# Performance work log

Measured on AMD Instinct MI355X. Metric: run time of the kernel, lower is better.

## Reference

```python
import jax, jax.numpy as jnp
import numpy as np
import math

D_MODEL = 1024
H = 16
D_K = D_MODEL // H
D_FF = 4096
NEG = -1e9


def layer_norm(x, alpha, bias):
    # Faithful to source: mean over last dim, UNBIASED std (torch.std default),
    # eps defined in source but never used in forward.
    mean = jnp.mean(x, axis=-1, keepdims=True)
    std = jnp.std(x, axis=-1, ddof=1, keepdims=True)
    return (x - mean) / std * alpha + bias


def mha(x, mask, w_q, w_k, w_v, w_o):
    B, S, D = x.shape
    q = (x @ w_q.T).reshape(B, S, H, D_K)
    k = (x @ w_k.T).reshape(B, S, H, D_K)
    v = (x @ w_v.T).reshape(B, S, H, D_K)
    scores = jnp.einsum('bqhd,bkhd->bhqk', q, k) / math.sqrt(D_K)
    scores = jnp.where(mask, NEG, scores)
    attn = jax.nn.softmax(scores, axis=-1)
    out = jnp.einsum('bhqk,bkhd->bqhd', attn, v).reshape(B, S, D)
    return out @ w_o.T


def setup_inputs() -> dict:
    key = jax.random.key(0)
    ks = jax.random.split(key, 16)
    B, S = 4, 2048
    s = 0.02
    return {
        'x': jax.random.normal(ks[0], (B, S, D_MODEL), jnp.float32),
        'w_q': jax.random.normal(ks[1], (D_MODEL, D_MODEL), jnp.float32) * s,
        'w_k': jax.random.normal(ks[2], (D_MODEL, D_MODEL), jnp.float32) * s,
        'w_v': jax.random.normal(ks[3], (D_MODEL, D_MODEL), jnp.float32) * s,
        'w_o': jax.random.normal(ks[4], (D_MODEL, D_MODEL), jnp.float32) * s,
        'l1_w': jax.random.normal(ks[5], (D_FF, D_MODEL), jnp.float32) * s,
        'l1_b': jnp.zeros((D_FF,), jnp.float32),
        'l2_w': jax.random.normal(ks[6], (D_MODEL, D_FF), jnp.float32) * s,
        'l2_b': jnp.zeros((D_MODEL,), jnp.float32),
        'norm1_a': jnp.ones((D_MODEL,), jnp.float32),
        'norm1_b': jnp.zeros((D_MODEL,), jnp.float32),
        'norm2_a': jnp.ones((D_MODEL,), jnp.float32),
        'norm2_b': jnp.zeros((D_MODEL,), jnp.float32),
        'normf_a': jnp.ones((D_MODEL,), jnp.float32),
        'normf_b': jnp.zeros((D_MODEL,), jnp.float32),
        'mask': jax.random.randint(ks[7], (B, 1, 1, S), 0, 2) == 1,
    }


def reference(x, w_q, w_k, w_v, w_o, l1_w, l1_b, l2_w, l2_b,
              norm1_a, norm1_b, norm2_a, norm2_b, normf_a, normf_b, mask):
    # residual 1: pre-norm self-attention (dropout is identity at eval)
    x = x + mha(layer_norm(x, norm1_a, norm1_b), mask, w_q, w_k, w_v, w_o)
    # residual 2: pre-norm FFN
    h = layer_norm(x, norm2_a, norm2_b)
    ff = jax.nn.relu(h @ l1_w.T + l1_b) @ l2_w.T + l2_b
    x = x + ff
    return layer_norm(x, normf_a, normf_b)
```

## Files before the change

kernel.cpp:

```cpp
#include <hip/hip_runtime.h>
#include <hip/hip_bf16.h>


typedef __bf16 bf16x8 __attribute__((ext_vector_type(8)));
typedef float f32x4 __attribute__((ext_vector_type(4)));
typedef unsigned short u16x8 __attribute__((ext_vector_type(8)));
using bf16 = __hip_bfloat16;

__device__ __forceinline__ f32x4 mfma16(bf16x8 a, bf16x8 b, f32x4 c) {
  return __builtin_amdgcn_mfma_f32_16x16x32_bf16(a, b, c, 0, 0, 0);
}

__device__ __forceinline__ int swz(int row, int blk) {
  return row * 64 + ((blk ^ (row & 7)) << 3);
}

__device__ __forceinline__ void stage_tile64(unsigned short* lds,
                                             const bf16* g, int ld, int rows) {
  const int lane = threadIdx.x & 63, wid = threadIdx.x >> 6;
  const int r8 = lane >> 3, blk = lane & 7;
  const bf16* gl = g + (size_t)r8 * ld + ((blk ^ r8) << 3);
  const int passes = rows >> 3;
  for (int p = wid; p < passes; p += 4) {
    __builtin_amdgcn_global_load_lds(
        (const __attribute__((address_space(1))) void*)(gl + (size_t)(p * 8) * ld),
        (__attribute__((address_space(3))) void*)(lds + p * 512),
        16, 0, 0);
  }
}

__device__ __forceinline__ short bfb(float x) {
  return (short)__hip_bfloat16_raw(__float2bfloat16(x)).x;
}

__global__ __launch_bounds__(256) void cvt_k(const float* __restrict__ s,
                                             bf16* __restrict__ d, int n) {
  const int i = (blockIdx.x * 256 + threadIdx.x) * 4;
  if (i + 3 < n) {
    const float4 v = *reinterpret_cast<const float4*>(s + i);
    ushort4 o;
    o.x = (unsigned short)bfb(v.x);
    o.y = (unsigned short)bfb(v.y);
    o.z = (unsigned short)bfb(v.z);
    o.w = (unsigned short)bfb(v.w);
    *reinterpret_cast<ushort4*>(d + i) = o;
  }
}

template <bool OUT_F32>
__global__ __launch_bounds__(256) void layernorm_k(const float* __restrict__ in,
                                                   const float* __restrict__ gamma,
                                                   const float* __restrict__ beta,
                                                   void* __restrict__ out) {
  __shared__ float red[8];
  const int row = blockIdx.x, t = threadIdx.x;
  const float4 vv = reinterpret_cast<const float4*>(in + (size_t)row * 1024)[t];
  const float x0 = vv.x, x1 = vv.y, x2 = vv.z, x3 = vv.w;
  float s = x0 + x1 + x2 + x3;
#pragma unroll
  for (int off = 32; off; off >>= 1) s += __shfl_down(s, off);
  if ((t & 63) == 0) red[t >> 6] = s;
  __syncthreads();
  const float mean = (red[0] + red[1] + red[2] + red[3]) * (1.0f / 1024.0f);
  const float d0 = x0 - mean, d1 = x1 - mean, d2 = x2 - mean, d3 = x3 - mean;
  float sq = d0 * d0 + d1 * d1 + d2 * d2 + d3 * d3;
#pragma unroll
  for (int off = 32; off; off >>= 1) sq += __shfl_down(sq, off);
  if ((t & 63) == 0) red[4 + (t >> 6)] = sq;
  __syncthreads();
  const float var =
      fmaxf((red[4] + red[5] + red[6] + red[7]) * (1.0f / 1023.0f), 1e-20f);
  const float rstd = rsqrtf(var);
  const float4 ga = reinterpret_cast<const float4*>(gamma)[t];
  const float4 be = reinterpret_cast<const float4*>(beta)[t];
  const float y0 = d0 * rstd * ga.x + be.x;
  const float y1 = d1 * rstd * ga.y + be.y;
  const float y2 = d2 * rstd * ga.z + be.z;
  const float y3 = d3 * rstd * ga.w + be.w;
  if (OUT_F32) {
    reinterpret_cast<float4*>((float*)out + (size_t)row * 1024)[t] =
        make_float4(y0, y1, y2, y3);
  } else {
    ushort4 o;
    o.x = (unsigned short)bfb(y0);
    o.y = (unsigned short)bfb(y1);
    o.z = (unsigned short)bfb(y2);
    o.w = (unsigned short)bfb(y3);
    reinterpret_cast<ushort4*>((bf16*)out + (size_t)row * 1024)[t] = o;
  }
}

template <bool HAS_BIAS, bool RELU, bool HAS_RES, bool OUT_F32>
__global__ __launch_bounds__(256) void gemm_bt(const bf16* __restrict__ A,
                                               const bf16* __restrict__ W,
                                               const float* __restrict__ bias,
                                               const float* __restrict__ resid,
                                               void* __restrict__ out,
                                               int M, int N, int K,
                                               int lda, int ldw) {
  __shared__ __align__(16) unsigned short As[128 * 64];
  __shared__ __align__(16) unsigned short Bs[128 * 64];
  const int lane = threadIdx.x & 63, wid = threadIdx.x >> 6;
  const int n16 = lane & 15, quad = lane >> 4;
  const int wm = (wid >> 1) * 64, wn = (wid & 1) * 64;
  const int tm = blockIdx.x * 128, tn = blockIdx.y * 128;
  f32x4 acc[4][4] = {};
  for (int k0 = 0; k0 < K; k0 += 64) {
    stage_tile64(As, A + (size_t)tm * lda + k0, lda, 128);
    stage_tile64(Bs, W + (size_t)tn * ldw + k0, ldw, 128);
    __syncthreads();
#pragma unroll
    for (int kk = 0; kk < 64; kk += 32) {
      bf16x8 af[4], bw[4];
#pragma unroll
      for (int i = 0; i < 4; ++i)
        af[i] = *reinterpret_cast<const bf16x8*>(
            &As[swz(wm + i * 16 + n16, (kk >> 3) + quad)]);
#pragma unroll
      for (int j = 0; j < 4; ++j)
        bw[j] = *reinterpret_cast<const bf16x8*>(
            &Bs[swz(wn + j * 16 + n16, (kk >> 3) + quad)]);
#pragma unroll
      for (int i = 0; i < 4; ++i)
#pragma unroll
        for (int j = 0; j < 4; ++j) acc[i][j] = mfma16(af[i], bw[j], acc[i][j]);
    }
    __syncthreads();
  }
#pragma unroll
  for (int i = 0; i < 4; ++i) {
#pragma unroll
    for (int j = 0; j < 4; ++j) {
      const int n = tn + wn + j * 16 + n16;
      const float bv = HAS_BIAS ? bias[n] : 0.0f;
#pragma unroll
      for (int r = 0; r < 4; ++r) {
        const int m = tm + wm + i * 16 + quad * 4 + r;
        float vv = acc[i][j][r] + bv;
        if (RELU) vv = fmaxf(vv, 0.0f);
        if (HAS_RES) vv += resid[(size_t)m * N + n];
        if (OUT_F32)
          ((float*)out)[(size_t)m * N + n] = vv;
        else
          ((bf16*)out)[(size_t)m * N + n] = __float2bfloat16(vv);
      }
    }
  }
}

__global__ __launch_bounds__(256) void prep_mask_k(const int* __restrict__ m,
                                                   float* __restrict__ mf,
                                                   int n) {
  __shared__ int s;
  if (threadIdx.x == 0) s = 0;
  __syncthreads();
  unsigned int acc = 0;
  for (int i = threadIdx.x; i < 512; i += 256)
    acc |= ((const unsigned int*)m)[i] & 0xFFFFFF00u;
  if (acc) atomicOr(&s, 1);
  __syncthreads();
  const bool bytes = (s != 0);
  const int i = blockIdx.x * 256 + threadIdx.x;
  if (i < n) {
    const int v = bytes ? (int)((const unsigned char*)m)[i] : m[i];
    mf[i] = v ? -1.4427e9f : 0.0f;
  }
}

__global__ __launch_bounds__(256) void scan_k(const float* __restrict__ maskf,
                                              float* __restrict__ cmask,
                                              int* __restrict__ idx,
                                              int* __restrict__ cnt) {
  __shared__ int wsum[4];
  const int b = blockIdx.x, t = threadIdx.x, lane = t & 63, w = t >> 6;
  const float* mrow = maskf + b * 2048;
  int keep[8], local = 0;
#pragma unroll
  for (int e = 0; e < 8; ++e) {
    keep[e] = (mrow[t * 8 + e] == 0.0f) ? 1 : 0;
    local += keep[e];
  }
  int inc = local;
#pragma unroll
  for (int off = 1; off < 64; off <<= 1) {
    int v = __shfl_up(inc, off);
    if (lane >= off) inc += v;
  }
  if (lane == 63) wsum[w] = inc;
  __syncthreads();
  int base = 0;
#pragma unroll
  for (int i = 0; i < 4; ++i)
    if (i < w) base += wsum[i];
  int p = base + inc - local;
#pragma unroll
  for (int e = 0; e < 8; ++e)
    if (keep[e]) idx[b * 2048 + p++] = t * 8 + e;
  const int total = wsum[0] + wsum[1] + wsum[2] + wsum[3];
  if (t == 0) cnt[b] = total;
  for (int i = t; i < 2048; i += 256)
    cmask[b * 2048 + i] = (i < total) ? 0.0f : -1.4427e9f;
}

__global__ __launch_bounds__(256) void gather_k(const bf16* __restrict__ qkv,
                                                const int* __restrict__ idx,
                                                const int* __restrict__ cnt,
                                                bf16* __restrict__ kv) {
  const int b = blockIdx.x >> 11, j = blockIdx.x & 2047;
  const int n = cnt[b];
  const int npad = (n + 63) & ~63;
  if (j >= npad) return;
  u16x8* dst = reinterpret_cast<u16x8*>(kv + ((size_t)(b * 2048 + j)) * 2048);
  if (j < n) {
    const int s = idx[b * 2048 + j];
    const u16x8* src = reinterpret_cast<const u16x8*>(
        qkv + ((size_t)(b * 2048 + s)) * 3072 + 1024);
    dst[threadIdx.x] = src[threadIdx.x];
  } else {
    u16x8 z = {};
    dst[threadIdx.x] = z;
  }
}

__global__ __launch_bounds__(256) void attn_k(const bf16* __restrict__ qkv,
                                              const bf16* __restrict__ kv,
                                              const float* __restrict__ cmask,
                                              const int* __restrict__ cnt,
                                              bf16* __restrict__ out, int BHN) {
  __shared__ __align__(16) unsigned short Ks[2][64 * 64];
  __shared__ __align__(16) unsigned short Vs[2][64 * 72];
  const int lane = threadIdx.x & 63, wid = threadIdx.x >> 6;
  const int n16 = lane & 15, quad = lane >> 4;
  const int bid = blockIdx.x;
  const int bh = bid % BHN, qb = bid / BHN;
  const int b = bh >> 4, h = bh & 15;
  const size_t rowb = (size_t)b * 2048 * 3072;
  const bf16* qp0 = qkv + rowb + h * 64;
  const bf16* kp0 = kv + (size_t)b * 2048 * 2048 + h * 64;
  const bf16* vp0 = kp0 + 1024;
  const float* mfb = cmask + b * 2048;
  const int nk = ((cnt[b] + 63) >> 6) << 6;
  const int qrow0 = qb * 128 + wid * 32;

  bf16x8 qf[2][2];
#pragma unroll
  for (int g = 0; g < 2; ++g) {
    const bf16* qp = qp0 + (size_t)(qrow0 + g * 16 + n16) * 3072 + quad * 8;
    qf[g][0] = *reinterpret_cast<const bf16x8*>(qp);
    qf[g][1] = *reinterpret_cast<const bf16x8*>(qp + 32);
  }
  bf16x8 ones;
#pragma unroll
  for (int e = 0; e < 8; ++e) ones[e] = (__bf16)1.0f;
  f32x4 oacc[2][4] = {};
  f32x4 lacc[2] = {};
  const int prow = ((n16 >> 2) << 3) + (n16 & 3);
  const int vkey = lane, vdc = wid * 16;

  stage_tile64(Ks[0], kp0, 2048, 64);
  {
    const bf16* vp = vp0 + (size_t)vkey * 2048 + vdc;
    const u16x8 a = *reinterpret_cast<const u16x8*>(vp);
    const u16x8 bq = *reinterpret_cast<const u16x8*>(vp + 8);
#pragma unroll
    for (int e = 0; e < 8; ++e) {
      Vs[0][(vdc + e) * 72 + vkey] = a[e];
      Vs[0][(vdc + 8 + e) * 72 + vkey] = bq[e];
    }
  }
  int cur = 0;
  for (int kt = 0; kt < nk; kt += 64) {
    __syncthreads();
    const bool hasNext = (kt + 64 < nk);
    u16x8 na = {}, nb = {};
    if (hasNext) {
      stage_tile64(Ks[cur ^ 1], kp0 + (size_t)(kt + 64) * 2048, 2048, 64);
      const bf16* vp = vp0 + (size_t)(kt + 64 + vkey) * 2048 + vdc;
      na = *reinterpret_cast<const u16x8*>(vp);
      nb = *reinterpret_cast<const u16x8*>(vp + 8);
    }
    const unsigned short* Kc = Ks[cur];
    const unsigned short* Vc = Vs[cur];
#pragma unroll
    for (int sub = 0; sub < 2; ++sub) {
      const int kb = sub * 32;
      bf16x8 aflo[2], afhi[2];
#pragma unroll
      for (int st = 0; st < 2; ++st) {
        const int row = kb + prow + st * 4;
        aflo[st] = *reinterpret_cast<const bf16x8*>(&Kc[swz(row, quad)]);
        afhi[st] = *reinterpret_cast<const bf16x8*>(&Kc[swz(row, 4 + quad)]);
      }
      __builtin_amdgcn_s_setprio(1);
      f32x4 z[2][2];
#pragma unroll
      for (int g = 0; g < 2; ++g)
#pragma unroll
        for (int st = 0; st < 2; ++st) {
          f32x4 zz = {};
          zz = mfma16(aflo[st], qf[g][0], zz);
          zz = mfma16(afhi[st], qf[g][1], zz);
          z[g][st] = zz;
        }
      __builtin_amdgcn_s_setprio(0);
      const float4 m0 =
          *reinterpret_cast<const float4*>(mfb + kt + kb + quad * 8);
      const float4 m1 =
          *reinterpret_cast<const float4*>(mfb + kt + kb + quad * 8 + 4);
      bf16x8 vf[4];
#pragma unroll
      for (int j = 0; j < 4; ++j)
        vf[j] = *reinterpret_cast<const bf16x8*>(
            &Vc[(j * 16 + n16) * 72 + kb + quad * 8]);
#pragma unroll
      for (int g = 0; g < 2; ++g) {
        bf16x8 pf;
#pragma unroll
        for (int r = 0; r < 4; ++r) {
          const float e0 = __builtin_amdgcn_exp2f(
              fmaf(z[g][0][r], 0.18033688f, ((const float*)&m0)[r]));
          const float e1 = __builtin_amdgcn_exp2f(
              fmaf(z[g][1][r], 0.18033688f, ((const float*)&m1)[r]));
          pf[r] = (__bf16)e0;
          pf[4 + r] = (__bf16)e1;
        }
        __builtin_amdgcn_s_setprio(1);
#pragma unroll
        for (int j = 0; j < 4; ++j) oacc[g][j] = mfma16(pf, vf[j], oacc[g][j]);
        lacc[g] = mfma16(pf, ones, lacc[g]);
        __builtin_amdgcn_s_setprio(0);
      }
    }
    if (hasNext) {
      unsigned short* Vn = Vs[cur ^ 1];
#pragma unroll
      for (int e = 0; e < 8; ++e) {
        Vn[(vdc + e) * 72 + vkey] = na[e];
        Vn[(vdc + 8 + e) * 72 + vkey] = nb[e];
      }
    }
    cur ^= 1;
  }
#pragma unroll
  for (int g = 0; g < 2; ++g) {
#pragma unroll
    for (int r = 0; r < 4; ++r) {
      const float lr = 1.0f / fmaxf(lacc[g][r], 1e-20f);
      bf16* op =
          out + (size_t)(b * 2048 + qrow0 + g * 16 + quad * 4 + r) * 1024 +
          h * 64;
#pragma unroll
      for (int j = 0; j < 4; ++j)
        op[j * 16 + n16] = __float2bfloat16(oacc[g][j][r] * lr);
    }
  }
}

extern "C" void kernel_launch(void* const* d_in, const int* in_sizes, int n_in,
                              void* d_out, int out_size, void* d_ws,
                              size_t ws_size, hipStream_t stream) {
  const float* x    = (const float*)d_in[0];
  const float* w_q  = (const float*)d_in[1];
  const float* w_k  = (const float*)d_in[2];
  const float* w_v  = (const float*)d_in[3];
  const float* w_o  = (const float*)d_in[4];
  const float* l1_w = (const float*)d_in[5];
  const float* l1_b = (const float*)d_in[6];
  const float* l2_w = (const float*)d_in[7];
  const float* l2_b = (const float*)d_in[8];
  const float* n1a  = (const float*)d_in[9];
  const float* n1b  = (const float*)d_in[10];
  const float* n2a  = (const float*)d_in[11];
  const float* n2b  = (const float*)d_in[12];
  const float* nfa  = (const float*)d_in[13];
  const float* nfb  = (const float*)d_in[14];
  const int* mask   = (const int*)d_in[15];

  const int D = 1024, FF = 4096;
  const int M = in_sizes[0] / D;
  const int B = M / 2048;

  const size_t MB = 1024ull * 1024ull;
  if (ws_size < 121 * MB) return;
  char* w = (char*)d_ws;
  bf16* WQKV = (bf16*)(w + 0 * MB);
  bf16* WO   = (bf16*)(w + 6 * MB);
  bf16* L1W  = (bf16*)(w + 8 * MB);
  bf16* L2W  = (bf16*)(w + 16 * MB);
  bf16* LN1  = (bf16*)(w + 24 * MB);
  bf16* QKV  = (bf16*)(w + 40 * MB);
  bf16* ATT  = LN1;
  bf16* HLN  = (bf16*)(w + 40 * MB);
  bf16* FF1  = (bf16*)(w + 56 * MB);
  bf16* KV   = (bf16*)(w + 88 * MB);
  float* X1  = (float*)(w + 88 * MB);
  float* MASKF = (float*)(w + 120 * MB);
  float* CMASK = (float*)(w + 120 * MB + 256 * 1024);
  int*   IDX   = (int*)(w + 120 * MB + 512 * 1024);
  int*   CNT   = (int*)(w + 120 * MB + 768 * 1024);

  const dim3 blk(256);
  cvt_k<<<dim3(D * D / 1024), blk, 0, stream>>>(w_q, WQKV, D * D);
  cvt_k<<<dim3(D * D / 1024), blk, 0, stream>>>(w_k, WQKV + D * D, D * D);
  cvt_k<<<dim3(D * D / 1024), blk, 0, stream>>>(w_v, WQKV + 2 * D * D, D * D);
  cvt_k<<<dim3(D * D / 1024), blk, 0, stream>>>(w_o, WO, D * D);
  cvt_k<<<dim3(FF * D / 1024), blk, 0, stream>>>(l1_w, L1W, FF * D);
  cvt_k<<<dim3(FF * D / 1024), blk, 0, stream>>>(l2_w, L2W, FF * D);
  prep_mask_k<<<dim3((M + 255) / 256), blk, 0, stream>>>(mask, MASKF, M);
  scan_k<<<dim3(B), blk, 0, stream>>>(MASKF, CMASK, IDX, CNT);

  layernorm_k<false><<<M, blk, 0, stream>>>(x, n1a, n1b, LN1);
  gemm_bt<false, false, false, false>
      <<<dim3(M / 128, 3072 / 128), blk, 0, stream>>>(LN1, WQKV, nullptr,
                                                      nullptr, QKV, M, 3072, D,
                                                      D, D);
  gather_k<<<dim3(B * 2048), blk, 0, stream>>>(QKV, IDX, CNT, KV);
  const int BHN = B * 16;
  attn_k<<<dim3((M / 128) * 16), blk, 0, stream>>>(QKV, KV, CMASK, CNT, ATT,
                                                   BHN);
  gemm_bt<false, false, true, true><<<dim3(M / 128, D / 128), blk, 0, stream>>>(
      ATT, WO, nullptr, x, X1, M, D, D, D, D);
  layernorm_k<false><<<M, blk, 0, stream>>>(X1, n2a, n2b, HLN);
  for (int c = 0; c < 2; ++c) {
    gemm_bt<true, true, false, false>
        <<<dim3(M / 128, 2048 / 128), blk, 0, stream>>>(
            HLN, L1W + (size_t)c * 2048 * D, l1_b + c * 2048, nullptr, FF1, M,
            2048, D, D, D);
    if (c == 0)
      gemm_bt<true, false, true, true>
          <<<dim3(M / 128, D / 128), blk, 0, stream>>>(
              FF1, L2W + c * 2048, l2_b, X1, X1, M, D, 2048, 2048, FF);
    else
      gemm_bt<false, false, true, true>
          <<<dim3(M / 128, D / 128), blk, 0, stream>>>(
              FF1, L2W + c * 2048, nullptr, X1, X1, M, D, 2048, 2048, FF);
  }
  layernorm_k<true><<<M, blk, 0, stream>>>(X1, nfa, nfb, (float*)d_out);
}
```

Before: 520.1 us.

## Gather unmasked LN rows before K/V projection and skip padded GEMM tiles

The fused QKV projection is split in two. Q is computed for all rows, while the layernormed input is first gathered to the unmasked key positions and only those rows go through the K/V GEMM. Workgroups whose rows fall past the padded count exit early, so masked keys never pay for the K/V projection. GEMM tiles are also remapped across groups of eight for locality, and attention skips the mask loads on fully valid key tiles. The cost is an extra kernel launch and a gather of LN rows, and the padding granularity changes to 128.

```diff
diff --git a/kernel.cpp b/kernel.cpp
--- a/kernel.cpp
+++ b/kernel.cpp
@@ -90,20 +90,34 @@
   }
 }
 
-template <bool HAS_BIAS, bool RELU, bool HAS_RES, bool OUT_F32>
+template <bool HAS_BIAS, bool RELU, bool HAS_RES, bool OUT_F32, bool KV_EXIT>
 __global__ __launch_bounds__(256) void gemm_bt(const bf16* __restrict__ A,
                                                const bf16* __restrict__ W,
                                                const float* __restrict__ bias,
                                                const float* __restrict__ resid,
                                                void* __restrict__ out,
                                                int M, int N, int K,
-                                               int lda, int ldw) {
+                                               int lda, int ldw,
+                                               const int* __restrict__ cnt) {
   __shared__ __align__(16) unsigned short As[128 * 64];
   __shared__ __align__(16) unsigned short Bs[128 * 64];
+  int bx = blockIdx.x, by = blockIdx.y;
+  const int nwg = gridDim.x * gridDim.y;
+  if ((nwg & 7) == 0) {
+    const int lid = by * gridDim.x + bx;
+    const int cpx = nwg >> 3;
+    const int s = (lid & 7) * cpx + (lid >> 3);
+    bx = s % gridDim.x;
+    by = s / gridDim.x;
+  }
+  const int tm = bx * 128, tn = by * 128;
+  if (KV_EXIT) {
+    const int npad = (cnt[tm >> 11] + 127) & ~127;
+    if ((tm & 2047) >= npad) return;
+  }
   const int lane = threadIdx.x & 63, wid = threadIdx.x >> 6;
   const int n16 = lane & 15, quad = lane >> 4;
   const int wm = (wid >> 1) * 64, wn = (wid & 1) * 64;
-  const int tm = blockIdx.x * 128, tn = blockIdx.y * 128;
   f32x4 acc[4][4] = {};
   for (int k0 = 0; k0 < K; k0 += 64) {
     stage_tile64(As, A + (size_t)tm * lda + k0, lda, 128);
@@ -202,19 +216,19 @@
     cmask[b * 2048 + i] = (i < total) ? 0.0f : -1.4427e9f;
 }
 
-__global__ __launch_bounds__(256) void gather_k(const bf16* __restrict__ qkv,
-                                                const int* __restrict__ idx,
-                                                const int* __restrict__ cnt,
-                                                bf16* __restrict__ kv) {
+__global__ __launch_bounds__(128) void gatherA_k(const bf16* __restrict__ ln1,
+                                                 const int* __restrict__ idx,
+                                                 const int* __restrict__ cnt,
+                                                 bf16* __restrict__ cln) {
   const int b = blockIdx.x >> 11, j = blockIdx.x & 2047;
   const int n = cnt[b];
-  const int npad = (n + 63) & ~63;
+  const int npad = (n + 127) & ~127;
   if (j >= npad) return;
-  u16x8* dst = reinterpret_cast<u16x8*>(kv + ((size_t)(b * 2048 + j)) * 2048);
+  u16x8* dst = reinterpret_cast<u16x8*>(cln + ((size_t)(b * 2048 + j)) * 1024);
   if (j < n) {
     const int s = idx[b * 2048 + j];
-    const u16x8* src = reinterpret_cast<const u16x8*>(
-        qkv + ((size_t)(b * 2048 + s)) * 3072 + 1024);
+    const u16x8* src =
+        reinterpret_cast<const u16x8*>(ln1 + ((size_t)(b * 2048 + s)) * 1024);
     dst[threadIdx.x] = src[threadIdx.x];
   } else {
     u16x8 z = {};
@@ -222,7 +236,7 @@
   }
 }
 
-__global__ __launch_bounds__(256) void attn_k(const bf16* __restrict__ qkv,
+__global__ __launch_bounds__(256) void attn_k(const bf16* __restrict__ q,
                                               const bf16* __restrict__ kv,
                                               const float* __restrict__ cmask,
                                               const int* __restrict__ cnt,
@@ -234,18 +248,18 @@
   const int bid = blockIdx.x;
   const int bh = bid % BHN, qb = bid / BHN;
   const int b = bh >> 4, h = bh & 15;
-  const size_t rowb = (size_t)b * 2048 * 3072;
-  const bf16* qp0 = qkv + rowb + h * 64;
+  const bf16* qp0 = q + (size_t)b * 2048 * 1024 + h * 64;
   const bf16* kp0 = kv + (size_t)b * 2048 * 2048 + h * 64;
   const bf16* vp0 = kp0 + 1024;
   const float* mfb = cmask + b * 2048;
-  const int nk = ((cnt[b] + 63) >> 6) << 6;
+  const int cntb = cnt[b];
+  const int nk = ((cntb + 63) >> 6) << 6;
   const int qrow0 = qb * 128 + wid * 32;
 
   bf16x8 qf[2][2];
 #pragma unroll
   for (int g = 0; g < 2; ++g) {
-    const bf16* qp = qp0 + (size_t)(qrow0 + g * 16 + n16) * 3072 + quad * 8;
+    const bf16* qp = qp0 + (size_t)(qrow0 + g * 16 + n16) * 1024 + quad * 8;
     qf[g][0] = *reinterpret_cast<const bf16x8*>(qp);
     qf[g][1] = *reinterpret_cast<const bf16x8*>(qp + 32);
   }
@@ -272,6 +286,7 @@
   for (int kt = 0; kt < nk; kt += 64) {
     __syncthreads();
     const bool hasNext = (kt + 64 < nk);
+    const bool fullTile = (kt + 64 <= cntb);
     u16x8 na = {}, nb = {};
     if (hasNext) {
       stage_tile64(Ks[cur ^ 1], kp0 + (size_t)(kt + 64) * 2048, 2048, 64);
@@ -303,10 +318,12 @@
           z[g][st] = zz;
         }
       __builtin_amdgcn_s_setprio(0);
-      const float4 m0 =
-          *reinterpret_cast<const float4*>(mfb + kt + kb + quad * 8);
-      const float4 m1 =
-          *reinterpret_cast<const float4*>(mfb + kt + kb + quad * 8 + 4);
+      float4 m0 = make_float4(0.f, 0.f, 0.f, 0.f);
+      float4 m1 = make_float4(0.f, 0.f, 0.f, 0.f);
+      if (!fullTile) {
+        m0 = *reinterpret_cast<const float4*>(mfb + kt + kb + quad * 8);
+        m1 = *reinterpret_cast<const float4*>(mfb + kt + kb + quad * 8 + 4);
+      }
       bf16x8 vf[4];
 #pragma unroll
       for (int j = 0; j < 4; ++j)
@@ -388,9 +405,10 @@
   bf16* L1W  = (bf16*)(w + 8 * MB);
   bf16* L2W  = (bf16*)(w + 16 * MB);
   bf16* LN1  = (bf16*)(w + 24 * MB);
-  bf16* QKV  = (bf16*)(w + 40 * MB);
+  bf16* Qbuf = (bf16*)(w + 40 * MB);
   bf16* ATT  = LN1;
   bf16* HLN  = (bf16*)(w + 40 * MB);
+  bf16* CLN  = (bf16*)(w + 56 * MB);
   bf16* FF1  = (bf16*)(w + 56 * MB);
   bf16* KV   = (bf16*)(w + 88 * MB);
   float* X1  = (float*)(w + 88 * MB);
@@ -410,30 +428,37 @@
   scan_k<<<dim3(B), blk, 0, stream>>>(MASKF, CMASK, IDX, CNT);
 
   layernorm_k<false><<<M, blk, 0, stream>>>(x, n1a, n1b, LN1);
-  gemm_bt<false, false, false, false>
-      <<<dim3(M / 128, 3072 / 128), blk, 0, stream>>>(LN1, WQKV, nullptr,
-                                                      nullptr, QKV, M, 3072, D,
-                                                      D, D);
-  gather_k<<<dim3(B * 2048), blk, 0, stream>>>(QKV, IDX, CNT, KV);
+  gemm_bt<false, false, false, false, false>
+      <<<dim3(M / 128, D / 128), blk, 0, stream>>>(LN1, WQKV, nullptr, nullptr,
+                                                   Qbuf, M, D, D, D, D,
+                                                   nullptr);
+  gatherA_k<<<dim3(B * 2048), dim3(128), 0, stream>>>(LN1, IDX, CNT, CLN);
+  gemm_bt<false, false, false, false, true>
+      <<<dim3(M / 128, 2048 / 128), blk, 0, stream>>>(
+          CLN, WQKV + (size_t)D * D, nullptr, nullptr, KV, M, 2048, D, D, D,
+          CNT);
   const int BHN = B * 16;
-  attn_k<<<dim3((M / 128) * 16), blk, 0, stream>>>(QKV, KV, CMASK, CNT, ATT,
+  attn_k<<<dim3((M / 128) * 16), blk, 0, stream>>>(Qbuf, KV, CMASK, CNT, ATT,
                                                    BHN);
-  gemm_bt<false, false, true, true><<<dim3(M / 128, D / 128), blk, 0, stream>>>(
-      ATT, WO, nullptr, x, X1, M, D, D, D, D);
+  gemm_bt<false, false, true, true, false>
+      <<<dim3(M / 128, D / 128), blk, 0, stream>>>(ATT, WO, nullptr, x, X1, M,
+                                                   D, D, D, D, nullptr);
   layernorm_k<false><<<M, blk, 0, stream>>>(X1, n2a, n2b, HLN);
   for (int c = 0; c < 2; ++c) {
-    gemm_bt<true, true, false, false>
+    gemm_bt<true, true, false, false, false>
         <<<dim3(M / 128, 2048 / 128), blk, 0, stream>>>(
             HLN, L1W + (size_t)c * 2048 * D, l1_b + c * 2048, nullptr, FF1, M,
-            2048, D, D, D);
+            2048, D, D, D, nullptr);
     if (c == 0)
-      gemm_bt<true, false, true, true>
+      gemm_bt<true, false, true, true, false>
           <<<dim3(M / 128, D / 128), blk, 0, stream>>>(
-              FF1, L2W + c * 2048, l2_b, X1, X1, M, D, 2048, 2048, FF);
+              FF1, L2W + c * 2048, l2_b, X1, X1, M, D, 2048, 2048, FF,
+              nullptr);
     else
-      gemm_bt<false, false, true, true>
+      gemm_bt<false, false, true, true, false>
           <<<dim3(M / 128, D / 128), blk, 0, stream>>>(
-              FF1, L2W + c * 2048, nullptr, X1, X1, M, D, 2048, 2048, FF);
+              FF1, L2W + c * 2048, nullptr, X1, X1, M, D, 2048, 2048, FF,
+              nullptr);
   }
   layernorm_k<true><<<M, blk, 0, stream>>>(X1, nfa, nfb, (float*)d_out);
 }
```

Measured after the change: 538.7 us. +3.6%, slower.
